# Performance work log

Hardware: AMD Instinct MI355X
Metric: run time of the kernel (lower is better)

Reference implementation:

```python
import jax, jax.numpy as jnp
import numpy as np

NUM_CODEBOOKS = 1
NUM_ENTRIES = 4096
ENTRY_DIM = 64


def setup_inputs() -> dict:
    key = jax.random.key(0)
    k1, k2 = jax.random.split(key)
    z = jax.random.normal(k1, (4, 1024, 8, 64), dtype=jnp.float32)
    weight = jax.random.normal(k2, (NUM_CODEBOOKS * NUM_ENTRIES, ENTRY_DIM), dtype=jnp.float32)
    return {"z": z, "weight": weight}


def _decode(z, weight):
    # Mirrors VQVAEQuantize.decode with cosine_distance=False.
    C, K, D = NUM_CODEBOOKS, NUM_ENTRIES, ENTRY_DIM
    input_shape = z.shape
    zf = z.reshape(-1, C, D).astype(jnp.float32)            # (N, C, D)
    cb = weight.reshape(C, K, D).astype(jnp.float32)        # (C, K, D)
    dots = jnp.einsum('ckd,ncd->cnk', cb, zf)               # (C, N, K)
    znorm = jnp.sum(zf * zf, axis=-1).T[:, :, None]         # (C, N, 1)
    cbnorm = jnp.sum(cb * cb, axis=-1)[:, None, :]          # (C, 1, K)
    sim = 2.0 * dots - znorm - cbnorm                        # negative squared dist
    idx = jnp.argmax(sim, axis=-1)                           # (C, N)
    idx = idx.T + jnp.arange(C, dtype=idx.dtype)[None, :] * K  # (N, C) global ids
    idx = idx.reshape(*input_shape[:-1], -1)
    z_q = weight[idx.reshape(-1)].reshape(input_shape)       # embedding gather
    return z_q, idx


def reference(z, weight):
    z_q, indices = _decode(z, weight)
    # commitment loss (training path): mse per (bsz, seq_len) position
    commitment_loss = ((z - jax.lax.stop_gradient(z_q)) ** 2)
    commitment_loss = commitment_loss.reshape(z.shape[0], z.shape[1], -1).mean(axis=-1)
    # codebook EMA statistics (update_codebook): one-hot scatter-add as segment_sum
    K_total = NUM_CODEBOOKS * NUM_ENTRIES
    flat_idx = indices.reshape(-1)
    encodings_sum = jax.ops.segment_sum(
        jnp.ones_like(flat_idx, dtype=jnp.float32), flat_idx, num_segments=K_total)
    embed_sum = jax.ops.segment_sum(
        z.reshape(-1, ENTRY_DIM), flat_idx, num_segments=K_total)
    # straight-through estimator (copy_grad=True)
    z_q = z + jax.lax.stop_gradient(z_q - z)
    return z_q, indices, commitment_loss, encodings_sum, embed_sum
```

## Files before the change

### kernel.cpp

```cpp
#include <hip/hip_runtime.h>
#include <math.h>

#define N_TOTAL   32768
#define K_ENT     4096
#define DIM       64
#define BMR       128
#define BK        128
#define CAPG      16
#define EPS       1.0f
#define BIAS      256.0f

typedef __attribute__((ext_vector_type(4))) float f32x4;
typedef __attribute__((ext_vector_type(8))) short bf16x8;
typedef __attribute__((ext_vector_type(4))) unsigned short u16x4;

#define WS_NCB    0
#define WS_WHI    4096
#define WS_RMX    135168
#define WS_CNT    167936
#define WS_CAND   200704
#define OUT_ZQ    0
#define OUT_IDX   2097152
#define OUT_LOSS  2129920
#define OUT_ENC   2134016
#define OUT_EMB   2138112

#define NEG_BIG   -3.0e38f

__device__ __forceinline__ float bf2f(unsigned short u) {
  return __uint_as_float(((unsigned int)u) << 16);
}
__device__ __forceinline__ unsigned short f2bf(float f) {
  unsigned int b = __float_as_uint(f);
  return (unsigned short)((b + 0x7fffu + ((b >> 16) & 1u)) >> 16);
}

__global__ __launch_bounds__(256) void prep_kernel(
    const float* __restrict__ w, unsigned short* __restrict__ whi,
    float* __restrict__ ncb) {
  int i = blockIdx.x * 256 + threadIdx.x;
  float4 v = ((const float4*)w)[i];
  u16x4 h;
  h[0] = f2bf(v.x); h[1] = f2bf(v.y); h[2] = f2bf(v.z); h[3] = f2bf(v.w);
  ((u16x4*)whi)[i] = h;
  float s = fmaf(v.x, v.x, fmaf(v.y, v.y, fmaf(v.z, v.z, v.w * v.w)));
  s += __shfl_xor(s, 1); s += __shfl_xor(s, 2);
  s += __shfl_xor(s, 4); s += __shfl_xor(s, 8);
  if ((threadIdx.x & 15) == 0) ncb[i >> 4] = BIAS - 0.5f * s;
}

__global__ __launch_bounds__(256, 2) void maxes_kernel(
    const float* __restrict__ z, const unsigned short* __restrict__ whi,
    const float* __restrict__ ncb, unsigned int* __restrict__ rmx) {
  const int tid = threadIdx.x;
  const int n0  = (blockIdx.x >> 1) * BMR;
  const int khalf = blockIdx.x & 1;
  const int st  = blockIdx.x & 15;
  const int wv  = tid >> 6;
  const int ln  = tid & 63;
  const int g   = ln >> 4;
  const int lm  = ln & 15;
  const int estripe = wv * 32;

  bf16x8 bz[8][2];
  #pragma unroll
  for (int rt = 0; rt < 8; ++rt) {
    const float* zr = z + (size_t)(n0 + rt * 16 + lm) * DIM;
    #pragma unroll
    for (int s = 0; s < 2; ++s) {
      float4 f0 = *(const float4*)(zr + s * 32 + g * 8);
      float4 f1 = *(const float4*)(zr + s * 32 + g * 8 + 4);
      float ff[8] = {f0.x, f0.y, f0.z, f0.w, f1.x, f1.y, f1.z, f1.w};
      bf16x8 h;
      #pragma unroll
      for (int i = 0; i < 8; ++i) h[i] = (short)f2bf(ff[i]);
      bz[rt][s] = h;
    }
  }

  float m[8];
  #pragma unroll
  for (int i = 0; i < 8; ++i) m[i] = NEG_BIG;

  bf16x8 awA[2][2], awB[2][2];
  float4 ncA[2], ncB[2];

  auto chunkbase = [&](int i) { return (khalf * 16 + ((i + st) & 15)) * BK; };
  auto loadW = [&](int kcb, bf16x8 (&aw)[2][2], float4 (&nc)[2]) {
    #pragma unroll
    for (int et = 0; et < 2; ++et) {
      const int ebase = kcb + estripe + et * 16;
      nc[et] = *(const float4*)(ncb + ebase + g * 4);
      const unsigned short* wr = whi + (size_t)(ebase + lm) * DIM + g * 8;
      aw[et][0] = *(const bf16x8*)(wr);
      aw[et][1] = *(const bf16x8*)(wr + 32);
    }
  };
  auto comp = [&](const bf16x8 (&aw)[2][2], const float4 (&nc)[2]) {
    f32x4 acc[2][8];
    #pragma unroll
    for (int et = 0; et < 2; ++et)
      #pragma unroll
      for (int rt = 0; rt < 8; ++rt)
        acc[et][rt] = (f32x4){nc[et].x, nc[et].y, nc[et].z, nc[et].w};
    #pragma unroll
    for (int et = 0; et < 2; ++et)
      #pragma unroll
      for (int s = 0; s < 2; ++s)
        #pragma unroll
        for (int rt = 0; rt < 8; ++rt)
          acc[et][rt] = __builtin_amdgcn_mfma_f32_16x16x32_bf16(
              aw[et][s], bz[rt][s], acc[et][rt], 0, 0, 0);
    #pragma unroll
    for (int rt = 0; rt < 8; ++rt) {
      float cm = fmaxf(
          fmaxf(fmaxf(acc[0][rt][0], acc[0][rt][1]),
                fmaxf(acc[0][rt][2], acc[0][rt][3])),
          fmaxf(fmaxf(acc[1][rt][0], acc[1][rt][1]),
                fmaxf(acc[1][rt][2], acc[1][rt][3])));
      m[rt] = fmaxf(m[rt], cm);
    }
  };

  loadW(chunkbase(0), awA, ncA);
  #pragma unroll 1
  for (int i = 0; i < 16; i += 2) {
    loadW(chunkbase(i + 1), awB, ncB);
    comp(awA, ncA);
    if (i + 2 < 16) loadW(chunkbase(i + 2), awA, ncA);
    comp(awB, ncB);
  }

  #pragma unroll
  for (int rt = 0; rt < 8; ++rt) {
    m[rt] = fmaxf(m[rt], __shfl_xor(m[rt], 16));
    m[rt] = fmaxf(m[rt], __shfl_xor(m[rt], 32));
  }
  if (ln < 16) {
    #pragma unroll
    for (int rt = 0; rt < 8; ++rt)
      atomicMax(&rmx[n0 + rt * 16 + ln], __float_as_uint(m[rt]));
  }
}

__global__ __launch_bounds__(256, 2) void collect_kernel(
    const float* __restrict__ z, const unsigned short* __restrict__ whi,
    const float* __restrict__ ncb, const unsigned int* __restrict__ rmx,
    int* __restrict__ cnt, int* __restrict__ cand) {
  const int tid = threadIdx.x;
  const int n0  = (blockIdx.x >> 1) * BMR;
  const int khalf = blockIdx.x & 1;
  const int st  = blockIdx.x & 15;
  const int wv  = tid >> 6;
  const int ln  = tid & 63;
  const int g   = ln >> 4;
  const int lm  = ln & 15;
  const int estripe = wv * 32;

  bf16x8 bz[8][2];
  #pragma unroll
  for (int rt = 0; rt < 8; ++rt) {
    const float* zr = z + (size_t)(n0 + rt * 16 + lm) * DIM;
    #pragma unroll
    for (int s = 0; s < 2; ++s) {
      float4 f0 = *(const float4*)(zr + s * 32 + g * 8);
      float4 f1 = *(const float4*)(zr + s * 32 + g * 8 + 4);
      float ff[8] = {f0.x, f0.y, f0.z, f0.w, f1.x, f1.y, f1.z, f1.w};
      bf16x8 h;
      #pragma unroll
      for (int i = 0; i < 8; ++i) h[i] = (short)f2bf(ff[i]);
      bz[rt][s] = h;
    }
  }

  float thr[8];
  #pragma unroll
  for (int rt = 0; rt < 8; ++rt)
    thr[rt] = __uint_as_float(rmx[n0 + rt * 16 + lm]) - EPS;

  bf16x8 awA[2][2], awB[2][2];
  float4 ncA[2], ncB[2];

  auto chunkbase = [&](int i) { return (khalf * 16 + ((i + st) & 15)) * BK; };
  auto loadW = [&](int kcb, bf16x8 (&aw)[2][2], float4 (&nc)[2]) {
    #pragma unroll
    for (int et = 0; et < 2; ++et) {
      const int ebase = kcb + estripe + et * 16;
      nc[et] = *(const float4*)(ncb + ebase + g * 4);
      const unsigned short* wr = whi + (size_t)(ebase + lm) * DIM + g * 8;
      aw[et][0] = *(const bf16x8*)(wr);
      aw[et][1] = *(const bf16x8*)(wr + 32);
    }
  };
  auto comp = [&](int kcb, const bf16x8 (&aw)[2][2], const float4 (&nc)[2]) {
    f32x4 acc[2][8];
    #pragma unroll
    for (int et = 0; et < 2; ++et)
      #pragma unroll
      for (int rt = 0; rt < 8; ++rt)
        acc[et][rt] = (f32x4){nc[et].x, nc[et].y, nc[et].z, nc[et].w};
    #pragma unroll
    for (int et = 0; et < 2; ++et)
      #pragma unroll
      for (int s = 0; s < 2; ++s)
        #pragma unroll
        for (int rt = 0; rt < 8; ++rt)
          acc[et][rt] = __builtin_amdgcn_mfma_f32_16x16x32_bf16(
              aw[et][s], bz[rt][s], acc[et][rt], 0, 0, 0);
    #pragma unroll
    for (int rt = 0; rt < 8; ++rt) {
      float hm = fmaxf(
          fmaxf(fmaxf(acc[0][rt][0], acc[0][rt][1]),
                fmaxf(acc[0][rt][2], acc[0][rt][3])),
          fmaxf(fmaxf(acc[1][rt][0], acc[1][rt][1]),
                fmaxf(acc[1][rt][2], acc[1][rt][3])));
      if (__builtin_expect(hm >= thr[rt], 0)) {
        const int rown = n0 + rt * 16 + lm;
        #pragma unroll
        for (int et = 0; et < 2; ++et)
          #pragma unroll
          for (int j = 0; j < 4; ++j) {
            if (acc[et][rt][j] >= thr[rt]) {
              int e = kcb + estripe + et * 16 + g * 4 + j;
              int p = atomicAdd(&cnt[rown], 1);
              if (p < CAPG) cand[rown * CAPG + p] = e;
            }
          }
      }
    }
  };

  loadW(chunkbase(0), awA, ncA);
  #pragma unroll 1
  for (int i = 0; i < 16; i += 2) {
    loadW(chunkbase(i + 1), awB, ncB);
    comp(chunkbase(i), awA, ncA);
    if (i + 2 < 16) loadW(chunkbase(i + 2), awA, ncA);
    comp(chunkbase(i + 1), awB, ncB);
  }
}

__global__ __launch_bounds__(512) void rescore_gather_kernel(
    const float* __restrict__ z, const float* __restrict__ w,
    const int* __restrict__ cnt, const int* __restrict__ cand,
    float* __restrict__ out_idx, float* __restrict__ out_zq,
    float* __restrict__ out_loss, float* __restrict__ enc,
    float* __restrict__ emb) {
  const int bs = blockIdx.x;
  const int tid = threadIdx.x;
  const int h = tid >> 6, d = tid & 63;
  const int n = bs * 8 + h;

  int nn = cnt[n];
  double bl = -1.0e300;
  int wl = 0x7fffffff;
  if (nn <= CAPG) {
    if (d < nn) {
      int c = cand[n * CAPG + d];
      double td = 0.0, ud = 0.0;
      #pragma unroll 8
      for (int d2 = 0; d2 < DIM; ++d2) {
        double wv = (double)w[(size_t)c * DIM + d2];
        double zv = (double)z[(size_t)n * DIM + d2];
        td = fma(zv, wv, td);
        ud = fma(wv, wv, ud);
      }
      bl = 2.0 * td - ud;
      wl = c;
    }
  } else {
    for (int t = 0; t < 64; ++t) {
      int c = t * 64 + d;
      double td = 0.0, ud = 0.0;
      for (int d2 = 0; d2 < DIM; ++d2) {
        double wv = (double)w[(size_t)c * DIM + d2];
        double zv = (double)z[(size_t)n * DIM + d2];
        td = fma(zv, wv, td);
        ud = fma(wv, wv, ud);
      }
      double sd = 2.0 * td - ud;
      if (sd > bl || (sd == bl && c < wl)) { bl = sd; wl = c; }
    }
  }
  #pragma unroll
  for (int mk = 1; mk <= 32; mk <<= 1) {
    double os = __shfl_xor(bl, mk);
    int   oi = __shfl_xor(wl, mk);
    if (os > bl || (os == bl && oi < wl)) { bl = os; wl = oi; }
  }
  int k = wl;
  k = (k < 0) ? 0 : ((k > K_ENT - 1) ? (K_ENT - 1) : k);
  if (d == 0) out_idx[n] = (float)k;

  const float zf = z[(size_t)n * DIM + d];
  float wvf = w[(size_t)k * DIM + d];
  float stv = zf + (wvf - zf);
  out_zq[(size_t)n * DIM + d] = stv;
  float diff = zf - wvf;
  float s = diff * diff;
  #pragma unroll
  for (int mm = 32; mm >= 1; mm >>= 1) s += __shfl_down(s, mm, 64);
  __shared__ float red[8];
  if ((tid & 63) == 0) red[tid >> 6] = s;
  __syncthreads();
  if (tid == 0) {
    float t = 0.f;
    #pragma unroll
    for (int i = 0; i < 8; ++i) t += red[i];
    out_loss[bs] = t * (1.0f / 512.0f);
  }
  atomicAdd(&emb[(size_t)k * DIM + d], zf);
  if (d == 0) atomicAdd(&enc[k], 1.0f);
}

extern "C" void kernel_launch(void* const* d_in, const int* in_sizes, int n_in,
                              void* d_out, int out_size, void* d_ws, size_t ws_size,
                              hipStream_t stream) {
  const float* z = (const float*)d_in[0];
  const float* w = (const float*)d_in[1];
  float* ws  = (float*)d_ws;
  float* ncb = ws + WS_NCB;
  unsigned short* whi = (unsigned short*)(ws + WS_WHI);
  unsigned int* rmx = (unsigned int*)(ws + WS_RMX);
  int* cnt  = (int*)(ws + WS_CNT);
  int* cand = (int*)(ws + WS_CAND);
  float* out = (float*)d_out;

  hipMemsetAsync(out + OUT_ENC, 0, (size_t)(4096 + 262144) * sizeof(float),
                 stream);
  hipMemsetAsync(rmx, 0, (size_t)(2 * N_TOTAL) * sizeof(int), stream);

  prep_kernel<<<(K_ENT * DIM / 4) / 256, 256, 0, stream>>>(w, whi, ncb);
  maxes_kernel<<<(N_TOTAL / BMR) * 2, 256, 0, stream>>>(z, whi, ncb, rmx);
  collect_kernel<<<(N_TOTAL / BMR) * 2, 256, 0, stream>>>(z, whi, ncb, rmx,
                                                          cnt, cand);
  rescore_gather_kernel<<<N_TOTAL / 8, 512, 0, stream>>>(
      z, w, cnt, cand, out + OUT_IDX, out + OUT_ZQ, out + OUT_LOSS,
      out + OUT_ENC, out + OUT_EMB);
}
```

Baseline: 126.0 us.

## Pre-pack codebook into MFMA fragment order, split K four ways, hand-scheduled loads

The prep kernel now writes the bf16 codebook in a packed layout that matches the per-lane MFMA fragment order, so each lane's global loads become contiguous dwordx4 reads. The maxes and collect kernels split the codebook into quarters instead of halves, doubling the grid to 1024 blocks. Weight loads are issued through inline asm with explicit vmcnt waits and scheduling barriers, so the prefetch overlaps the MFMA work. The extra blocks mean each block re-converts its z tile and issues more atomics, and the hand-written wait counts depend on a fixed load order.

```diff
diff --git a/kernel.cpp b/kernel.cpp
--- a/kernel.cpp
+++ b/kernel.cpp
@@ -27,6 +27,11 @@
 
 #define NEG_BIG   -3.0e38f
 
+#define GLOAD(dst, ptr) \
+  asm volatile("global_load_dwordx4 %0, %1, off" : "=&v"(dst) : "v"(ptr))
+#define VMWAIT(n) asm volatile("s_waitcnt vmcnt(" #n ")")
+#define SB0() __builtin_amdgcn_sched_barrier(0)
+
 __device__ __forceinline__ float bf2f(unsigned short u) {
   return __uint_as_float(((unsigned int)u) << 16);
 }
@@ -36,26 +41,34 @@
 }
 
 __global__ __launch_bounds__(256) void prep_kernel(
-    const float* __restrict__ w, unsigned short* __restrict__ whi,
+    const float* __restrict__ w, unsigned short* __restrict__ whiP,
     float* __restrict__ ncb) {
   int i = blockIdx.x * 256 + threadIdx.x;
   float4 v = ((const float4*)w)[i];
   u16x4 h;
   h[0] = f2bf(v.x); h[1] = f2bf(v.y); h[2] = f2bf(v.z); h[3] = f2bf(v.w);
-  ((u16x4*)whi)[i] = h;
-  float s = fmaf(v.x, v.x, fmaf(v.y, v.y, fmaf(v.z, v.z, v.w * v.w)));
-  s += __shfl_xor(s, 1); s += __shfl_xor(s, 2);
-  s += __shfl_xor(s, 4); s += __shfl_xor(s, 8);
-  if ((threadIdx.x & 15) == 0) ncb[i >> 4] = BIAS - 0.5f * s;
+  const int e   = i >> 4;
+  const int us  = (i & 15) * 4;
+  const int s   = us >> 5;
+  const int w32 = us & 31;
+  const int g   = w32 >> 3;
+  const int rem = w32 & 7;
+  const int ln  = g * 16 + (e & 15);
+  const size_t pidx = ((size_t)((e >> 4) * 2 + s) * 64 + ln) * 8 + rem;
+  *(u16x4*)(whiP + pidx) = h;
+  float sq = fmaf(v.x, v.x, fmaf(v.y, v.y, fmaf(v.z, v.z, v.w * v.w)));
+  sq += __shfl_xor(sq, 1); sq += __shfl_xor(sq, 2);
+  sq += __shfl_xor(sq, 4); sq += __shfl_xor(sq, 8);
+  if ((threadIdx.x & 15) == 0) ncb[i >> 4] = BIAS - 0.5f * sq;
 }
 
 __global__ __launch_bounds__(256, 2) void maxes_kernel(
-    const float* __restrict__ z, const unsigned short* __restrict__ whi,
+    const float* __restrict__ z, const unsigned short* __restrict__ whiP,
     const float* __restrict__ ncb, unsigned int* __restrict__ rmx) {
   const int tid = threadIdx.x;
-  const int n0  = (blockIdx.x >> 1) * BMR;
-  const int khalf = blockIdx.x & 1;
-  const int st  = blockIdx.x & 15;
+  const int n0  = (blockIdx.x >> 2) * BMR;
+  const int kq  = blockIdx.x & 3;
+  const int st  = blockIdx.x & 7;
   const int wv  = tid >> 6;
   const int ln  = tid & 63;
   const int g   = ln >> 4;
@@ -83,26 +96,27 @@
   for (int i = 0; i < 8; ++i) m[i] = NEG_BIG;
 
   bf16x8 awA[2][2], awB[2][2];
-  float4 ncA[2], ncB[2];
-
-  auto chunkbase = [&](int i) { return (khalf * 16 + ((i + st) & 15)) * BK; };
-  auto loadW = [&](int kcb, bf16x8 (&aw)[2][2], float4 (&nc)[2]) {
+  f32x4  ncA[2], ncB[2];
+
+  auto chunkbase = [&](int i) { return (kq * 8 + ((i + st) & 7)) * BK; };
+  auto loadW = [&](int kcb, bf16x8 (&aw)[2][2], f32x4 (&nc)[2]) {
     #pragma unroll
     for (int et = 0; et < 2; ++et) {
       const int ebase = kcb + estripe + et * 16;
-      nc[et] = *(const float4*)(ncb + ebase + g * 4);
-      const unsigned short* wr = whi + (size_t)(ebase + lm) * DIM + g * 8;
-      aw[et][0] = *(const bf16x8*)(wr);
-      aw[et][1] = *(const bf16x8*)(wr + 32);
+      const unsigned short* wrp =
+          whiP + ((size_t)(ebase >> 4) * 2) * 512 + (size_t)ln * 8;
+      GLOAD(aw[et][0], wrp);
+      GLOAD(aw[et][1], wrp + 512);
+      GLOAD(nc[et], ncb + ebase + g * 4);
     }
   };
-  auto comp = [&](const bf16x8 (&aw)[2][2], const float4 (&nc)[2]) {
+  auto comp = [&](const bf16x8 (&aw)[2][2], const f32x4 (&nc)[2]) {
     f32x4 acc[2][8];
     #pragma unroll
     for (int et = 0; et < 2; ++et)
       #pragma unroll
       for (int rt = 0; rt < 8; ++rt)
-        acc[et][rt] = (f32x4){nc[et].x, nc[et].y, nc[et].z, nc[et].w};
+        acc[et][rt] = (f32x4){nc[et][0], nc[et][1], nc[et][2], nc[et][3]};
     #pragma unroll
     for (int et = 0; et < 2; ++et)
       #pragma unroll
@@ -124,10 +138,17 @@
 
   loadW(chunkbase(0), awA, ncA);
   #pragma unroll 1
-  for (int i = 0; i < 16; i += 2) {
+  for (int i = 0; i < 8; i += 2) {
     loadW(chunkbase(i + 1), awB, ncB);
+    VMWAIT(6); SB0();
     comp(awA, ncA);
-    if (i + 2 < 16) loadW(chunkbase(i + 2), awA, ncA);
+    if (i + 2 < 8) {
+      loadW(chunkbase(i + 2), awA, ncA);
+      VMWAIT(6);
+    } else {
+      VMWAIT(0);
+    }
+    SB0();
     comp(awB, ncB);
   }
 
@@ -144,13 +165,13 @@
 }
 
 __global__ __launch_bounds__(256, 2) void collect_kernel(
-    const float* __restrict__ z, const unsigned short* __restrict__ whi,
+    const float* __restrict__ z, const unsigned short* __restrict__ whiP,
     const float* __restrict__ ncb, const unsigned int* __restrict__ rmx,
     int* __restrict__ cnt, int* __restrict__ cand) {
   const int tid = threadIdx.x;
-  const int n0  = (blockIdx.x >> 1) * BMR;
-  const int khalf = blockIdx.x & 1;
-  const int st  = blockIdx.x & 15;
+  const int n0  = (blockIdx.x >> 2) * BMR;
+  const int kq  = blockIdx.x & 3;
+  const int st  = blockIdx.x & 7;
   const int wv  = tid >> 6;
   const int ln  = tid & 63;
   const int g   = ln >> 4;
@@ -179,26 +200,27 @@
     thr[rt] = __uint_as_float(rmx[n0 + rt * 16 + lm]) - EPS;
 
   bf16x8 awA[2][2], awB[2][2];
-  float4 ncA[2], ncB[2];
-
-  auto chunkbase = [&](int i) { return (khalf * 16 + ((i + st) & 15)) * BK; };
-  auto loadW = [&](int kcb, bf16x8 (&aw)[2][2], float4 (&nc)[2]) {
+  f32x4  ncA[2], ncB[2];
+
+  auto chunkbase = [&](int i) { return (kq * 8 + ((i + st) & 7)) * BK; };
+  auto loadW = [&](int kcb, bf16x8 (&aw)[2][2], f32x4 (&nc)[2]) {
     #pragma unroll
     for (int et = 0; et < 2; ++et) {
       const int ebase = kcb + estripe + et * 16;
-      nc[et] = *(const float4*)(ncb + ebase + g * 4);
-      const unsigned short* wr = whi + (size_t)(ebase + lm) * DIM + g * 8;
-      aw[et][0] = *(const bf16x8*)(wr);
-      aw[et][1] = *(const bf16x8*)(wr + 32);
+      const unsigned short* wrp =
+          whiP + ((size_t)(ebase >> 4) * 2) * 512 + (size_t)ln * 8;
+      GLOAD(aw[et][0], wrp);
+      GLOAD(aw[et][1], wrp + 512);
+      GLOAD(nc[et], ncb + ebase + g * 4);
     }
   };
-  auto comp = [&](int kcb, const bf16x8 (&aw)[2][2], const float4 (&nc)[2]) {
+  auto comp = [&](int kcb, const bf16x8 (&aw)[2][2], const f32x4 (&nc)[2]) {
     f32x4 acc[2][8];
     #pragma unroll
     for (int et = 0; et < 2; ++et)
       #pragma unroll
       for (int rt = 0; rt < 8; ++rt)
-        acc[et][rt] = (f32x4){nc[et].x, nc[et].y, nc[et].z, nc[et].w};
+        acc[et][rt] = (f32x4){nc[et][0], nc[et][1], nc[et][2], nc[et][3]};
     #pragma unroll
     for (int et = 0; et < 2; ++et)
       #pragma unroll
@@ -232,10 +254,17 @@
 
   loadW(chunkbase(0), awA, ncA);
   #pragma unroll 1
-  for (int i = 0; i < 16; i += 2) {
+  for (int i = 0; i < 8; i += 2) {
     loadW(chunkbase(i + 1), awB, ncB);
+    VMWAIT(6); SB0();
     comp(chunkbase(i), awA, ncA);
-    if (i + 2 < 16) loadW(chunkbase(i + 2), awA, ncA);
+    if (i + 2 < 8) {
+      loadW(chunkbase(i + 2), awA, ncA);
+      VMWAIT(6);
+    } else {
+      VMWAIT(0);
+    }
+    SB0();
     comp(chunkbase(i + 1), awB, ncB);
   }
 }
@@ -320,7 +349,7 @@
   const float* w = (const float*)d_in[1];
   float* ws  = (float*)d_ws;
   float* ncb = ws + WS_NCB;
-  unsigned short* whi = (unsigned short*)(ws + WS_WHI);
+  unsigned short* whiP = (unsigned short*)(ws + WS_WHI);
   unsigned int* rmx = (unsigned int*)(ws + WS_RMX);
   int* cnt  = (int*)(ws + WS_CNT);
   int* cand = (int*)(ws + WS_CAND);
@@ -330,9 +359,9 @@
                  stream);
   hipMemsetAsync(rmx, 0, (size_t)(2 * N_TOTAL) * sizeof(int), stream);
 
-  prep_kernel<<<(K_ENT * DIM / 4) / 256, 256, 0, stream>>>(w, whi, ncb);
-  maxes_kernel<<<(N_TOTAL / BMR) * 2, 256, 0, stream>>>(z, whi, ncb, rmx);
-  collect_kernel<<<(N_TOTAL / BMR) * 2, 256, 0, stream>>>(z, whi, ncb, rmx,
+  prep_kernel<<<(K_ENT * DIM / 4) / 256, 256, 0, stream>>>(w, whiP, ncb);
+  maxes_kernel<<<(N_TOTAL / BMR) * 4, 256, 0, stream>>>(z, whiP, ncb, rmx);
+  collect_kernel<<<(N_TOTAL / BMR) * 4, 256, 0, stream>>>(z, whiP, ncb, rmx,
                                                           cnt, cand);
   rescore_gather_kernel<<<N_TOTAL / 8, 512, 0, stream>>>(
       z, w, cnt, cand, out + OUT_IDX, out + OUT_ZQ, out + OUT_LOSS,
```

Result: slower. 132.2 us (+4.9%).
